# Performance work log

Measured on AMD Instinct MI355X. Metric: run time of the kernel, lower is better.

Reference implementation:

```python
import jax, jax.numpy as jnp
import numpy as np

N = 100000   # nodes
E = 1000000  # edges
IN, HID, OUT = 128, 64, 64


def setup_inputs() -> dict:
    key = jax.random.key(0)
    ks = jax.random.split(key, 6)
    x = jax.random.normal(ks[0], (N, IN), dtype=jnp.float32)
    edge_index = jax.random.randint(ks[1], (2, E), 0, N, dtype=jnp.int64)
    edge_attr = jax.random.uniform(ks[2], (E,), dtype=jnp.float32)
    # Glorot-style init like PyG GCNConv (weight [in, out], bias zeros)
    W1 = jax.random.normal(ks[3], (IN, HID), dtype=jnp.float32) * (1.0 / np.sqrt(IN))
    b1 = jnp.zeros((HID,), dtype=jnp.float32)
    W2 = jax.random.normal(ks[4], (HID, OUT), dtype=jnp.float32) * (1.0 / np.sqrt(HID))
    b2 = jnp.zeros((OUT,), dtype=jnp.float32)
    return {"x": x, "edge_index": edge_index, "edge_attr": edge_attr,
            "W1": W1, "b1": b1, "W2": W2, "b2": b2}


def gcn_conv(x, edge_index, edge_weight, W, b):
    """GCNConv: add self-loops, symmetric normalization, linear + scatter-add."""
    n = x.shape[0]
    row, col = edge_index[0], edge_index[1]
    loop = jnp.arange(n, dtype=row.dtype)
    row = jnp.concatenate([row, loop])
    col = jnp.concatenate([col, loop])
    w = jnp.concatenate([edge_weight, jnp.ones((n,), dtype=x.dtype)])
    deg = jax.ops.segment_sum(w, col, num_segments=n)              # [N]
    dinv = jnp.where(deg > 0, jax.lax.rsqrt(deg), 0.0)
    norm = dinv[row] * w * dinv[col]                               # [E+N]
    h = x @ W                                                      # [N, out]
    agg = jax.ops.segment_sum(h[row] * norm[:, None], col, num_segments=n)
    return agg + b


def reference(x, edge_index, edge_attr, W1, b1, W2, b2):
    h = jax.nn.relu(gcn_conv(x, edge_index, edge_attr, W1, b1))
    return jax.nn.relu(gcn_conv(h, edge_index, edge_attr, W2, b2))
```

## Files before the change

### kernel.cpp

```cpp
#include <hip/hip_runtime.h>


#define BNODES 512
#define LB 9
#define MAXBKT 256
#define EPT 12
#define EPB (256 * EPT)

typedef __attribute__((ext_vector_type(8))) short bf16x8;
typedef __attribute__((ext_vector_type(8))) unsigned short u16x8;
typedef __attribute__((ext_vector_type(8))) float f32x8;
typedef __attribute__((ext_vector_type(4))) float f32x4;

__device__ __forceinline__ unsigned short f2bf(float f) {
    unsigned u = __float_as_uint(f);
    u = (u + 0x7FFF + ((u >> 16) & 1)) >> 16;
    return (unsigned short)u;
}
__device__ __forceinline__ float bf2f(unsigned short h) {
    return __uint_as_float(((unsigned)h) << 16);
}
__device__ __forceinline__ f32x8 bf8tof(u16x8 u) {
    f32x8 r;
    #pragma unroll
    for (int i = 0; i < 8; ++i) r[i] = bf2f(u[i]);
    return r;
}

__device__ __forceinline__ int waveIncScan(int v, int lane) {
    #pragma unroll
    for (int d = 1; d < 64; d <<= 1) {
        int u = __shfl_up(v, d, 64);
        if (lane >= d) v += u;
    }
    return v;
}

template<int NW>
__device__ __forceinline__ int blockIncScan(int v, int t, int* wt) {
    int lane = t & 63, w = t >> 6;
    int s = waveIncScan(v, lane);
    if (lane == 63) wt[w] = s;
    __syncthreads();
    int add = 0;
    #pragma unroll
    for (int i = 0; i < NW - 1; ++i) if (i < w) add += wt[i];
    return s + add;
}

__device__ __forceinline__ f32x8 gather8(
    const unsigned short* __restrict__ G, const int2* __restrict__ sedge,
    int s, int m, int p8, f32x8 a0)
{
    f32x8 a1 = (f32x8)0.f;
    int e = s, e_end = s + m;
    if ((((unsigned long long)(sedge + e)) & 8) && e < e_end) {
        int2 pk = sedge[e++];
        float w = __int_as_float(pk.y);
        a0 += w * bf8tof(*(const u16x8*)&G[(size_t)pk.x * 64 + p8 * 8]);
    }
    for (; e + 1 < e_end; e += 2) {
        int4 pp = *(const int4*)&sedge[e];
        float w0 = __int_as_float(pp.y);
        float w1 = __int_as_float(pp.w);
        u16x8 g0 = *(const u16x8*)&G[(size_t)pp.x * 64 + p8 * 8];
        u16x8 g1 = *(const u16x8*)&G[(size_t)pp.z * 64 + p8 * 8];
        a0 += w0 * bf8tof(g0);
        a1 += w1 * bf8tof(g1);
    }
    if (e < e_end) {
        int2 pk = sedge[e];
        float w = __int_as_float(pk.y);
        a0 += w * bf8tof(*(const u16x8*)&G[(size_t)pk.x * 64 + p8 * 8]);
    }
    return a0 + a1;
}


__global__ __launch_bounds__(256) void hist_kernel(
    const int* __restrict__ col, int* __restrict__ H, int E, int NBKT,
    const float* __restrict__ W1, const float* __restrict__ W2,
    unsigned short* __restrict__ WT1, unsigned short* __restrict__ WT2, int NEB)
{
    int t = threadIdx.x, blk = blockIdx.x;
    if (blk >= NEB) {
        int i = (blk - NEB) * 256 + t;
        if (i < 64 * 128) {
            int c = i >> 7, k = i & 127;
            WT1[i] = f2bf(W1[k * 64 + c]);
        } else if (i < 64 * 128 + 64 * 64) {
            int j = i - 64 * 128;
            int c = j >> 6, k = j & 63;
            WT2[j] = f2bf(W2[k * 64 + c]);
        }
        return;
    }
    __shared__ int h[MAXBKT];
    for (int b = t; b < NBKT; b += 256) h[b] = 0;
    __syncthreads();
    int base = blk * EPB;
    #pragma unroll
    for (int i = 0; i < EPT; ++i) {
        int e = base + i * 256 + t;
        if (e < E) atomicAdd(&h[col[e] >> LB], 1);
    }
    __syncthreads();
    for (int b = t; b < NBKT; b += 256) H[blk * NBKT + b] = h[b];
}

__global__ __launch_bounds__(512) void rowscan_kernel(
    int* __restrict__ H, int* __restrict__ rowSum, int NEB, int NBKT)
{
    __shared__ int wt[8];
    int b = blockIdx.x, t = threadIdx.x;
    int v = (t < NEB) ? H[t * NBKT + b] : 0;
    int incl = blockIncScan<8>(v, t, wt);
    if (t < NEB) H[t * NBKT + b] = incl - v;
    if (t == 511) rowSum[b] = incl;
}

__global__ __launch_bounds__(256) void scatter_gemm_kernel(
    const int* __restrict__ row, const int* __restrict__ col,
    const float* __restrict__ w, const int* __restrict__ H,
    const int* __restrict__ rowSum, int2* __restrict__ sedge1,
    int E, int NBKT, int NEB,
    const float* __restrict__ X, const unsigned short* __restrict__ WT,
    unsigned short* __restrict__ G, int n)
{
    __shared__ __align__(16) char smem[32768];
    const int t = threadIdx.x;
    const int blk = blockIdx.x;

    if (blk < NEB) {
        int2* stage = (int2*)smem;
        unsigned char* bstage = (unsigned char*)(stage + EPB);
        int* lcnt  = (int*)(bstage + EPB);
        int* loff  = lcnt + MAXBKT;
        int* lcur  = loff + MAXBKT;
        int* gbase = lcur + MAXBKT;
        int* wt    = gbase + MAXBKT;

        int vb = (t < NBKT) ? rowSum[t] : 0;
        int ib = blockIncScan<4>(vb, t, wt);
        if (t < NBKT) gbase[t] = (ib - vb) + H[blk * NBKT + t];
        for (int b = t; b < NBKT; b += 256) lcnt[b] = 0;
        __syncthreads();

        int base = blk * EPB;
        #pragma unroll
        for (int i = 0; i < EPT; ++i) {
            int e = base + i * 256 + t;
            if (e < E) atomicAdd(&lcnt[col[e] >> LB], 1);
        }
        __syncthreads();
        int v = (t < NBKT) ? lcnt[t] : 0;
        int incl = blockIncScan<4>(v, t, wt);
        if (t < NBKT) {
            int x0 = incl - v;
            loff[t] = x0;
            lcur[t] = x0;
        }
        __syncthreads();
        #pragma unroll
        for (int i = 0; i < EPT; ++i) {
            int e = base + i * 256 + t;
            if (e < E) {
                int c = col[e];
                int b = c >> LB;
                int pos = atomicAdd(&lcur[b], 1);
                int2 pk;
                pk.x = row[e] | ((c & (BNODES - 1)) << 20);
                pk.y = __float_as_int(w[e]);
                stage[pos] = pk;
                bstage[pos] = (unsigned char)b;
            }
        }
        __syncthreads();
        int ecnt = E - base; if (ecnt > EPB) ecnt = EPB;
        for (int i = t; i < ecnt; i += 256) {
            int b = bstage[i];
            int g = gbase[b] + (i - loff[b]);
            sedge1[g] = stage[i];
        }
        return;
    }

    constexpr int K = 128, ROWB = 256, SLOTS = 16, CPR = 32;
    char* xs = smem;
    char* ws = smem + 64 * ROWB;
    const int nodeBase = (blk - NEB) * 64;

    for (int q = t; q < 64 * SLOTS; q += 256) {
        int r = q / SLOTS, s = q % SLOTS;
        uint4 v = *(const uint4*)(WT + r * K + s * 8);
        *(uint4*)(ws + r * ROWB + ((s ^ (r & 7)) * 16)) = v;
    }
    for (int q = t; q < 64 * CPR; q += 256) {
        int r = q / CPR, c = q % CPR;
        int node = nodeBase + r;
        float4 v = make_float4(0.f, 0.f, 0.f, 0.f);
        if (node < n) v = *(const float4*)(X + (size_t)node * K + c * 4);
        ushort4 h;
        h.x = f2bf(v.x); h.y = f2bf(v.y); h.z = f2bf(v.z); h.w = f2bf(v.w);
        *(ushort4*)(xs + r * ROWB + (((c >> 1) ^ (r & 7)) * 16) + (c & 1) * 8) = h;
    }
    __syncthreads();

    const int lane = t & 63;
    const int wv = t >> 6;
    const int lr = lane & 15;
    const int lk = lane >> 4;
    const int arow = (wv << 4) + lr;

    f32x4 acc[4] = {};
    #pragma unroll
    for (int kb = 0; kb < 4; ++kb) {
        int s = kb * 4 + lk;
        bf16x8 a = *(bf16x8*)(xs + arow * ROWB + ((s ^ (arow & 7)) * 16));
        #pragma unroll
        for (int cb = 0; cb < 4; ++cb) {
            int c = cb * 16 + lr;
            bf16x8 b = *(bf16x8*)(ws + c * ROWB + ((s ^ (c & 7)) * 16));
            acc[cb] = __builtin_amdgcn_mfma_f32_16x16x32_bf16(a, b, acc[cb], 0, 0, 0);
        }
    }

    int rowbase = nodeBase + (wv << 4) + (lk << 2);
    #pragma unroll
    for (int j = 0; j < 4; ++j) {
        int node = rowbase + j;
        if (node >= n) continue;
        #pragma unroll
        for (int cb = 0; cb < 4; ++cb)
            G[(size_t)node * 64 + cb * 16 + lr] = f2bf(acc[cb][j]);
    }
}

__global__ __launch_bounds__(512) void fine_dinv_kernel(
    const int2* __restrict__ sedge1, const int* __restrict__ rowSum,
    int* __restrict__ nodeStart, int* __restrict__ nodeCnt,
    float* __restrict__ dinv, int n, int NBKT)
{
    __shared__ int cnt[BNODES];
    __shared__ float wsum[BNODES];
    __shared__ int bs[MAXBKT + 1];
    __shared__ int wt[8];
    int b = blockIdx.x, t = threadIdx.x;

    int vb = (t < NBKT) ? rowSum[t] : 0;
    int ib = blockIncScan<8>(vb, t, wt);
    if (t < NBKT) bs[t] = ib - vb;
    if (t == 511) bs[NBKT] = ib;
    cnt[t] = 0; wsum[t] = 1.0f;
    __syncthreads();

    int s = bs[b], e = bs[b + 1];
    for (int j = s + t; j < e; j += 512) {
        int2 pk = sedge1[j];
        int ld = pk.x >> 20;
        atomicAdd(&cnt[ld], 1);
        atomicAdd(&wsum[ld], __int_as_float(pk.y));
    }
    __syncthreads();
    int v = cnt[t];
    int incl = blockIncScan<8>(v, t, wt);
    int x0 = s + incl - v;
    int node = b * BNODES + t;
    if (node < n) {
        nodeStart[node] = x0;
        nodeCnt[node] = v;
        dinv[node] = rsqrtf(wsum[t]);
    }
}

__global__ __launch_bounds__(512) void fine_csr_kernel(
    const int2* __restrict__ sedge1, const int* __restrict__ rowSum,
    const int* __restrict__ nodeStart, const float* __restrict__ dinv,
    int2* __restrict__ sedge2, int n, int NBKT)
{
    __shared__ int cur[BNODES];
    __shared__ float dloc[BNODES];
    __shared__ int bs[MAXBKT + 1];
    __shared__ int wt[8];
    int b = blockIdx.x, t = threadIdx.x;

    int vb = (t < NBKT) ? rowSum[t] : 0;
    int ib = blockIncScan<8>(vb, t, wt);
    if (t < NBKT) bs[t] = ib - vb;
    if (t == 511) bs[NBKT] = ib;
    int node = b * BNODES + t;
    cur[t]  = (node < n) ? nodeStart[node] : 0;
    dloc[t] = (node < n) ? dinv[node] : 0.f;
    __syncthreads();

    int s = bs[b], e = bs[b + 1];
    for (int j = s + t; j < e; j += 512) {
        int2 pk = sedge1[j];
        int ld = pk.x >> 20;
        int rw = pk.x & 0xFFFFF;
        int pos = atomicAdd(&cur[ld], 1);
        float wp = __int_as_float(pk.y) * dinv[rw] * dloc[ld];
        sedge2[pos] = make_int2(rw, __float_as_int(wp));
    }
}

__global__ __launch_bounds__(256) void aggmm_kernel(
    const unsigned short* __restrict__ G1, const int2* __restrict__ sedge2,
    const int* __restrict__ nodeStart, const int* __restrict__ nodeCnt,
    const float* __restrict__ dinv, const float* __restrict__ bias,
    const unsigned short* __restrict__ WT2, unsigned short* __restrict__ G2, int n)
{
    constexpr int BN = 32;
    constexpr int ROWB = 128;
    __shared__ char smem[(BN + 64) * ROWB];
    char* xs = smem;
    char* ws = smem + BN * ROWB;
    const int tid = threadIdx.x;
    const int nodeBase = blockIdx.x * BN;

    for (int q = tid; q < 64 * 8; q += 256) {
        int r = q >> 3, s = q & 7;
        uint4 v = *(const uint4*)(WT2 + r * 64 + s * 8);
        *(uint4*)(ws + r * ROWB + ((s ^ (r & 7)) * 16)) = v;
    }

    int p8 = tid & 7;
    int r = tid >> 3;
    int node = nodeBase + r;
    f32x8 o = (f32x8)0.f;
    if (node < n) {
        float di = dinv[node];
        f32x8 a = (di * di) * bf8tof(*(const u16x8*)&G1[(size_t)node * 64 + p8 * 8]);
        a = gather8(G1, sedge2, nodeStart[node], nodeCnt[node], p8, a);
        #pragma unroll
        for (int i = 0; i < 8; ++i)
            o[i] = fmaxf(a[i] + bias[p8 * 8 + i], 0.f);
    }
    u16x8 h;
    #pragma unroll
    for (int i = 0; i < 8; ++i) h[i] = f2bf(o[i]);
    *(u16x8*)(xs + r * ROWB + ((p8 ^ (r & 7)) * 16)) = h;
    __syncthreads();

    const int lane = tid & 63;
    const int w = tid >> 6;
    const int lr = lane & 15;
    const int lk = lane >> 4;
    const int rb = w >> 1;
    const int arow = rb * 16 + lr;

    f32x4 acc[2] = {};
    #pragma unroll
    for (int kb = 0; kb < 2; ++kb) {
        int s = kb * 4 + lk;
        bf16x8 a = *(bf16x8*)(xs + arow * ROWB + ((s ^ (arow & 7)) * 16));
        #pragma unroll
        for (int cc = 0; cc < 2; ++cc) {
            int c = ((w & 1) * 2 + cc) * 16 + lr;
            bf16x8 b = *(bf16x8*)(ws + c * ROWB + ((s ^ (c & 7)) * 16));
            acc[cc] = __builtin_amdgcn_mfma_f32_16x16x32_bf16(a, b, acc[cc], 0, 0, 0);
        }
    }

    int rowbase = nodeBase + rb * 16 + (lk << 2);
    #pragma unroll
    for (int j = 0; j < 4; ++j) {
        int nd = rowbase + j;
        if (nd >= n) continue;
        #pragma unroll
        for (int cc = 0; cc < 2; ++cc)
            G2[(size_t)nd * 64 + ((w & 1) * 2 + cc) * 16 + lr] = f2bf(acc[cc][j]);
    }
}

__global__ __launch_bounds__(256) void agg_kernel(
    const unsigned short* __restrict__ G, const int2* __restrict__ sedge2,
    const int* __restrict__ nodeStart, const int* __restrict__ nodeCnt,
    const float* __restrict__ dinv, const float* __restrict__ bias,
    float* __restrict__ OUT, int n)
{
    int t = blockIdx.x * blockDim.x + threadIdx.x;
    if (t >= n * 8) return;
    int node = t >> 3, p8 = t & 7;

    float di = dinv[node];
    f32x8 a = (di * di) * bf8tof(*(const u16x8*)&G[(size_t)node * 64 + p8 * 8]);
    a = gather8(G, sedge2, nodeStart[node], nodeCnt[node], p8, a);

    float4 o0, o1;
    o0.x = fmaxf(a[0] + bias[p8 * 8 + 0], 0.f);
    o0.y = fmaxf(a[1] + bias[p8 * 8 + 1], 0.f);
    o0.z = fmaxf(a[2] + bias[p8 * 8 + 2], 0.f);
    o0.w = fmaxf(a[3] + bias[p8 * 8 + 3], 0.f);
    o1.x = fmaxf(a[4] + bias[p8 * 8 + 4], 0.f);
    o1.y = fmaxf(a[5] + bias[p8 * 8 + 5], 0.f);
    o1.z = fmaxf(a[6] + bias[p8 * 8 + 6], 0.f);
    o1.w = fmaxf(a[7] + bias[p8 * 8 + 7], 0.f);
    *(float4*)&OUT[(size_t)node * 64 + p8 * 8] = o0;
    *(float4*)&OUT[(size_t)node * 64 + p8 * 8 + 4] = o1;
}

extern "C" void kernel_launch(void* const* d_in, const int* in_sizes, int n_in,
                              void* d_out, int out_size, void* d_ws, size_t ws_size,
                              hipStream_t stream) {
    const float* x     = (const float*)d_in[0];
    const int*   eidx  = (const int*)d_in[1];
    const float* eattr = (const float*)d_in[2];
    const float* W1    = (const float*)d_in[3];
    const float* b1    = (const float*)d_in[4];
    const float* W2    = (const float*)d_in[5];
    const float* b2    = (const float*)d_in[6];
    float* out = (float*)d_out;

    const int n = in_sizes[0] / 128;
    const int E = in_sizes[2];
    const int* row = eidx;
    const int* col = eidx + E;

    const int NBKT = (n + BNODES - 1) / BNODES;
    const int NEB  = (E + EPB - 1) / EPB;

    int2*  sedge1 = (int2*)d_ws;
    int2*  sedge2 = sedge1 + (size_t)E;
    unsigned short* g1 = (unsigned short*)(sedge2 + (size_t)E);
    unsigned short* g2 = g1 + (size_t)n * 64;
    unsigned short* WT1 = g2 + (size_t)n * 64;
    unsigned short* WT2 = WT1 + 64 * 128;
    float* dinv      = (float*)(WT2 + 64 * 64);
    int*   nodeStart = (int*)(dinv + n);
    int*   nodeCnt   = nodeStart + n;
    int*   H         = nodeCnt + n;
    int*   rowSum    = H + (size_t)NEB * NBKT;

    const int nbG  = (n + 63) / 64;
    const int nbG2 = (n + 31) / 32;
    const int nbA8 = (int)(((size_t)n * 8 + 255) / 256);

    hist_kernel<<<NEB + 48, 256, 0, stream>>>(col, H, E, NBKT, W1, W2, WT1, WT2, NEB);
    rowscan_kernel<<<NBKT, 512, 0, stream>>>(H, rowSum, NEB, NBKT);
    scatter_gemm_kernel<<<NEB + nbG, 256, 0, stream>>>(
        row, col, eattr, H, rowSum, sedge1, E, NBKT, NEB, x, WT1, g1, n);
    fine_dinv_kernel<<<NBKT, 512, 0, stream>>>(sedge1, rowSum, nodeStart, nodeCnt,
                                               dinv, n, NBKT);
    fine_csr_kernel<<<NBKT, 512, 0, stream>>>(sedge1, rowSum, nodeStart, dinv,
                                              sedge2, n, NBKT);

    aggmm_kernel<<<nbG2, 256, 0, stream>>>(g1, sedge2, nodeStart, nodeCnt, dinv, b1, WT2, g2, n);
    agg_kernel<<<nbA8, 256, 0, stream>>>(g2, sedge2, nodeStart, nodeCnt, dinv, b2, out, n);
}
```

Measured before the change: 109.0 us.

## Split bf16 feature tables into 16-column planes for cache-local gathers

Stores the intermediate bf16 feature matrices G1/G2 as four planes of 16 columns each (plane-major) instead of row-major 64 columns. The final aggregation kernel is reorganised so each block processes one plane for 128 nodes, so the gathered working set per plane (about 3.2 MB) can stay in L2 while random neighbour rows are fetched. The cost is that edge lists are read four times in agg_kernel and each gather fetches only 32 bytes per row. aggmm keeps its old thread mapping and still touches all planes.

```diff
diff --git a/kernel.cpp b/kernel.cpp
--- a/kernel.cpp
+++ b/kernel.cpp
@@ -48,30 +48,30 @@
     return s + add;
 }
 
-__device__ __forceinline__ f32x8 gather8(
-    const unsigned short* __restrict__ G, const int2* __restrict__ sedge,
-    int s, int m, int p8, f32x8 a0)
+__device__ __forceinline__ f32x8 gather8p(
+    const unsigned short* __restrict__ Gp, const int2* __restrict__ sedge,
+    int s, int m, int off8, f32x8 a0)
 {
     f32x8 a1 = (f32x8)0.f;
     int e = s, e_end = s + m;
     if ((((unsigned long long)(sedge + e)) & 8) && e < e_end) {
         int2 pk = sedge[e++];
         float w = __int_as_float(pk.y);
-        a0 += w * bf8tof(*(const u16x8*)&G[(size_t)pk.x * 64 + p8 * 8]);
+        a0 += w * bf8tof(*(const u16x8*)&Gp[(size_t)pk.x * 16 + off8]);
     }
     for (; e + 1 < e_end; e += 2) {
         int4 pp = *(const int4*)&sedge[e];
         float w0 = __int_as_float(pp.y);
         float w1 = __int_as_float(pp.w);
-        u16x8 g0 = *(const u16x8*)&G[(size_t)pp.x * 64 + p8 * 8];
-        u16x8 g1 = *(const u16x8*)&G[(size_t)pp.z * 64 + p8 * 8];
+        u16x8 g0 = *(const u16x8*)&Gp[(size_t)pp.x * 16 + off8];
+        u16x8 g1 = *(const u16x8*)&Gp[(size_t)pp.z * 16 + off8];
         a0 += w0 * bf8tof(g0);
         a1 += w1 * bf8tof(g1);
     }
     if (e < e_end) {
         int2 pk = sedge[e];
         float w = __int_as_float(pk.y);
-        a0 += w * bf8tof(*(const u16x8*)&G[(size_t)pk.x * 64 + p8 * 8]);
+        a0 += w * bf8tof(*(const u16x8*)&Gp[(size_t)pk.x * 16 + off8]);
     }
     return a0 + a1;
 }
@@ -125,7 +125,7 @@
     const int* __restrict__ rowSum, int2* __restrict__ sedge1,
     int E, int NBKT, int NEB,
     const float* __restrict__ X, const unsigned short* __restrict__ WT,
-    unsigned short* __restrict__ G, int n)
+    unsigned short* __restrict__ G, int n, int np16)
 {
     __shared__ __align__(16) char smem[32768];
     const int t = threadIdx.x;
@@ -232,7 +232,7 @@
         if (node >= n) continue;
         #pragma unroll
         for (int cb = 0; cb < 4; ++cb)
-            G[(size_t)node * 64 + cb * 16 + lr] = f2bf(acc[cb][j]);
+            G[(size_t)cb * np16 + (size_t)node * 16 + lr] = f2bf(acc[cb][j]);
     }
 }
 
@@ -308,7 +308,8 @@
     const unsigned short* __restrict__ G1, const int2* __restrict__ sedge2,
     const int* __restrict__ nodeStart, const int* __restrict__ nodeCnt,
     const float* __restrict__ dinv, const float* __restrict__ bias,
-    const unsigned short* __restrict__ WT2, unsigned short* __restrict__ G2, int n)
+    const unsigned short* __restrict__ WT2, unsigned short* __restrict__ G2,
+    int n, int np16)
 {
     constexpr int BN = 32;
     constexpr int ROWB = 128;
@@ -327,11 +328,13 @@
     int p8 = tid & 7;
     int r = tid >> 3;
     int node = nodeBase + r;
+    const unsigned short* Gp = G1 + (size_t)(p8 >> 1) * np16;
+    const int off8 = (p8 & 1) * 8;
     f32x8 o = (f32x8)0.f;
     if (node < n) {
         float di = dinv[node];
-        f32x8 a = (di * di) * bf8tof(*(const u16x8*)&G1[(size_t)node * 64 + p8 * 8]);
-        a = gather8(G1, sedge2, nodeStart[node], nodeCnt[node], p8, a);
+        f32x8 a = (di * di) * bf8tof(*(const u16x8*)&Gp[(size_t)node * 16 + off8]);
+        a = gather8p(Gp, sedge2, nodeStart[node], nodeCnt[node], off8, a);
         #pragma unroll
         for (int i = 0; i < 8; ++i)
             o[i] = fmaxf(a[i] + bias[p8 * 8 + i], 0.f);
@@ -368,8 +371,10 @@
         int nd = rowbase + j;
         if (nd >= n) continue;
         #pragma unroll
-        for (int cc = 0; cc < 2; ++cc)
-            G2[(size_t)nd * 64 + ((w & 1) * 2 + cc) * 16 + lr] = f2bf(acc[cc][j]);
+        for (int cc = 0; cc < 2; ++cc) {
+            int plane = (w & 1) * 2 + cc;
+            G2[(size_t)plane * np16 + (size_t)nd * 16 + lr] = f2bf(acc[cc][j]);
+        }
     }
 }
 
@@ -377,27 +382,32 @@
     const unsigned short* __restrict__ G, const int2* __restrict__ sedge2,
     const int* __restrict__ nodeStart, const int* __restrict__ nodeCnt,
     const float* __restrict__ dinv, const float* __restrict__ bias,
-    float* __restrict__ OUT, int n)
-{
-    int t = blockIdx.x * blockDim.x + threadIdx.x;
-    if (t >= n * 8) return;
-    int node = t >> 3, p8 = t & 7;
+    float* __restrict__ OUT, int n, int np16, int NBN)
+{
+    int p  = blockIdx.x / NBN;
+    int nb = blockIdx.x % NBN;
+    int node = nb * 128 + (threadIdx.x >> 1);
+    if (node >= n) return;
+    int h = threadIdx.x & 1;
+    const int off8 = h * 8;
+    const unsigned short* Gp = G + (size_t)p * np16;
 
     float di = dinv[node];
-    f32x8 a = (di * di) * bf8tof(*(const u16x8*)&G[(size_t)node * 64 + p8 * 8]);
-    a = gather8(G, sedge2, nodeStart[node], nodeCnt[node], p8, a);
-
+    f32x8 a = (di * di) * bf8tof(*(const u16x8*)&Gp[(size_t)node * 16 + off8]);
+    a = gather8p(Gp, sedge2, nodeStart[node], nodeCnt[node], off8, a);
+
+    int fb = p * 16 + off8;
     float4 o0, o1;
-    o0.x = fmaxf(a[0] + bias[p8 * 8 + 0], 0.f);
-    o0.y = fmaxf(a[1] + bias[p8 * 8 + 1], 0.f);
-    o0.z = fmaxf(a[2] + bias[p8 * 8 + 2], 0.f);
-    o0.w = fmaxf(a[3] + bias[p8 * 8 + 3], 0.f);
-    o1.x = fmaxf(a[4] + bias[p8 * 8 + 4], 0.f);
-    o1.y = fmaxf(a[5] + bias[p8 * 8 + 5], 0.f);
-    o1.z = fmaxf(a[6] + bias[p8 * 8 + 6], 0.f);
-    o1.w = fmaxf(a[7] + bias[p8 * 8 + 7], 0.f);
-    *(float4*)&OUT[(size_t)node * 64 + p8 * 8] = o0;
-    *(float4*)&OUT[(size_t)node * 64 + p8 * 8 + 4] = o1;
+    o0.x = fmaxf(a[0] + bias[fb + 0], 0.f);
+    o0.y = fmaxf(a[1] + bias[fb + 1], 0.f);
+    o0.z = fmaxf(a[2] + bias[fb + 2], 0.f);
+    o0.w = fmaxf(a[3] + bias[fb + 3], 0.f);
+    o1.x = fmaxf(a[4] + bias[fb + 4], 0.f);
+    o1.y = fmaxf(a[5] + bias[fb + 5], 0.f);
+    o1.z = fmaxf(a[6] + bias[fb + 6], 0.f);
+    o1.w = fmaxf(a[7] + bias[fb + 7], 0.f);
+    *(float4*)&OUT[(size_t)node * 64 + fb] = o0;
+    *(float4*)&OUT[(size_t)node * 64 + fb + 4] = o1;
 }
 
 extern "C" void kernel_launch(void* const* d_in, const int* in_sizes, int n_in,
@@ -419,6 +429,7 @@
 
     const int NBKT = (n + BNODES - 1) / BNODES;
     const int NEB  = (E + EPB - 1) / EPB;
+    const int np16 = n * 16;
 
     int2*  sedge1 = (int2*)d_ws;
     int2*  sedge2 = sedge1 + (size_t)E;
@@ -434,17 +445,19 @@
 
     const int nbG  = (n + 63) / 64;
     const int nbG2 = (n + 31) / 32;
-    const int nbA8 = (int)(((size_t)n * 8 + 255) / 256);
+    const int NBN  = (n + 127) / 128;
 
     hist_kernel<<<NEB + 48, 256, 0, stream>>>(col, H, E, NBKT, W1, W2, WT1, WT2, NEB);
     rowscan_kernel<<<NBKT, 512, 0, stream>>>(H, rowSum, NEB, NBKT);
     scatter_gemm_kernel<<<NEB + nbG, 256, 0, stream>>>(
-        row, col, eattr, H, rowSum, sedge1, E, NBKT, NEB, x, WT1, g1, n);
+        row, col, eattr, H, rowSum, sedge1, E, NBKT, NEB, x, WT1, g1, n, np16);
     fine_dinv_kernel<<<NBKT, 512, 0, stream>>>(sedge1, rowSum, nodeStart, nodeCnt,
                                                dinv, n, NBKT);
     fine_csr_kernel<<<NBKT, 512, 0, stream>>>(sedge1, rowSum, nodeStart, dinv,
                                               sedge2, n, NBKT);
 
-    aggmm_kernel<<<nbG2, 256, 0, stream>>>(g1, sedge2, nodeStart, nodeCnt, dinv, b1, WT2, g2, n);
-    agg_kernel<<<nbA8, 256, 0, stream>>>(g2, sedge2, nodeStart, nodeCnt, dinv, b2, out, n);
-}
+    aggmm_kernel<<<nbG2, 256, 0, stream>>>(g1, sedge2, nodeStart, nodeCnt, dinv,
+                                           b1, WT2, g2, n, np16);
+    agg_kernel<<<4 * NBN, 256, 0, stream>>>(g2, sedge2, nodeStart, nodeCnt, dinv,
+                                            b2, out, n, np16, NBN);
+}
```

After: 187.4 us. 1.72x slower.
